# Performance work log

Measured on AMD Instinct MI355X. Metric: run time of the kernel, lower is better.

The kernel has to match this reference:

```python
import jax, jax.numpy as jnp
import numpy as np
import math

N_HEADS, INPUT_DIM, EMBED_DIM = 8, 128, 128
KEY_DIM = EMBED_DIM // N_HEADS  # val_dim = key_dim = 16
B, N = 4, 512


def setup_inputs() -> dict:
    key = jax.random.key(0)
    ks = jax.random.split(key, 8)
    stdv_k = 1.0 / math.sqrt(KEY_DIM)
    stdv_e = 1.0 / math.sqrt(EMBED_DIM)
    stdv_1 = 1.0
    q = jax.random.normal(ks[0], (B, N, INPUT_DIM), dtype=jnp.float32)
    e = jax.random.normal(ks[1], (B, N, N, INPUT_DIM), dtype=jnp.float32)
    W_query = jax.random.uniform(ks[2], (N_HEADS, INPUT_DIM, KEY_DIM), jnp.float32, -stdv_k, stdv_k)
    W_key = jax.random.uniform(ks[3], (N_HEADS, INPUT_DIM, KEY_DIM), jnp.float32, -stdv_k, stdv_k)
    W_val = jax.random.uniform(ks[4], (N_HEADS, INPUT_DIM, KEY_DIM), jnp.float32, -stdv_k, stdv_k)
    E_val1 = jax.random.uniform(ks[5], (N_HEADS, INPUT_DIM, 1), jnp.float32, -stdv_1, stdv_1)
    W_out = jax.random.uniform(ks[6], (N_HEADS, KEY_DIM, EMBED_DIM), jnp.float32, -stdv_e, stdv_e)
    return {"q": q, "e": e, "W_query": W_query, "W_key": W_key,
            "W_val": W_val, "E_val1": E_val1, "W_out": W_out}


def reference(q, e, W_query, W_key, W_val, E_val1, W_out):
    # h = q (self-attention); shapes: q [B,N,D], e [B,N,N,D]
    norm = 1.0 / math.sqrt(W_query.shape[-1])
    Q = jnp.einsum('bnd,hdk->hbnk', q, W_query)  # [H,B,N,k]
    K = jnp.einsum('bnd,hdk->hbnk', q, W_key)
    V = jnp.einsum('bnd,hdv->hbnv', q, W_val)
    # edge bias: per-head scalar projection of edge features -> [H,B,N,N]
    E = jnp.einsum('bnmd,hd->hbnm', e, E_val1[..., 0])
    compat = norm * jnp.einsum('hbnk,hbmk->hbnm', Q, K) + E
    attn = jax.nn.softmax(compat, axis=-1)
    heads = jnp.einsum('hbnm,hbmv->hbnv', attn, V)
    out = jnp.einsum('hbnv,hve->bne', heads, W_out)  # [B,N,embed]
    return out
```

## Files before the change

### kernel.cpp

```cpp
#include <hip/hip_runtime.h>
#include <math.h>

#define BB 4
#define NN 512
#define DD 128
#define HH 8
#define KK 16

typedef float f4 __attribute__((ext_vector_type(4)));

__device__ __forceinline__ f4 ntload4(const float* p) {
    return __builtin_nontemporal_load(reinterpret_cast<const f4*>(p));
}

__global__ __launch_bounds__(128) void proj_kernel(
    const float* __restrict__ q,
    const float* __restrict__ Wq,
    const float* __restrict__ Wk,
    const float* __restrict__ Wv,
    float* __restrict__ Qs,
    float* __restrict__ Kp,
    float* __restrict__ Vp)
{
    __shared__ float qrow[DD];
    const int bn = blockIdx.x;
    const int t = threadIdx.x;
    qrow[t] = q[(size_t)bn * DD + t];
    __syncthreads();
    const int h = t >> 4;
    const int k = t & 15;
    const float* wq = Wq + (size_t)h * DD * KK + k;
    const float* wk = Wk + (size_t)h * DD * KK + k;
    const float* wv = Wv + (size_t)h * DD * KK + k;
    float aq = 0.f, ak = 0.f, av = 0.f;
#pragma unroll 16
    for (int d = 0; d < DD; ++d) {
        const float x = qrow[d];
        aq = fmaf(x, wq[(size_t)d * KK], aq);
        ak = fmaf(x, wk[(size_t)d * KK], ak);
        av = fmaf(x, wv[(size_t)d * KK], av);
    }
    Qs[(size_t)bn * DD + t] = aq * 0.25f;
    Kp[(size_t)bn * DD + t] = ak;
    Vp[(size_t)bn * DD + t] = av;
}

__global__ __launch_bounds__(256) void vt_kernel(
    const float* __restrict__ Vp, float* __restrict__ Vt)
{
    __shared__ float tile[64][129];
    const int b  = blockIdx.x >> 3;
    const int m0 = (blockIdx.x & 7) * 64;
    const int t  = threadIdx.x;
    const float* src = Vp + ((size_t)b * NN + m0) * DD;
#pragma unroll
    for (int j = 0; j < 8; ++j) {
        const int idx4 = t + j * 256;
        const float4 v = *(const float4*)(src + (size_t)idx4 * 4);
        const int r = idx4 >> 5, c = (idx4 & 31) * 4;
        tile[r][c] = v.x; tile[r][c+1] = v.y; tile[r][c+2] = v.z; tile[r][c+3] = v.w;
    }
    __syncthreads();
    const int m = t & 63;
#pragma unroll
    for (int p0 = 0; p0 < 128; p0 += 4) {
        const int p = p0 + (t >> 6);
        Vt[((size_t)b * DD + p) * NN + m0 + m] = tile[m][p];
    }
}

__global__ __launch_bounds__(256) void qkt_kernel(
    const float* __restrict__ Qs, const float* __restrict__ Kp,
    float* __restrict__ QKT)
{
    const int b    = blockIdx.x >> 7;
    const int n4   = blockIdx.x & 127;
    const int tid  = threadIdx.x;
    const int wave = tid >> 6;
    const int lane = tid & 63;
    const int sub  = lane >> 4;
    const int dc   = lane & 15;
    const int d0   = dc * 8;

    float qf[4][8];
#pragma unroll
    for (int j = 0; j < 4; ++j) {
        const float* qp = Qs + ((size_t)b * NN + n4 * 4 + j) * DD + d0;
        const float4 a = *(const float4*)qp;
        const float4 c = *(const float4*)(qp + 4);
        qf[j][0]=a.x; qf[j][1]=a.y; qf[j][2]=a.z; qf[j][3]=a.w;
        qf[j][4]=c.x; qf[j][5]=c.y; qf[j][6]=c.z; qf[j][7]=c.w;
    }
    const float* kbase = Kp + (size_t)b * NN * DD;
    for (int i = 0; i < 32; ++i) {
        const int m = wave * 128 + i * 4 + sub;
        const float* kp = kbase + (size_t)m * DD + d0;
        const float4 k0 = *(const float4*)kp;
        const float4 k1 = *(const float4*)(kp + 4);
        float kr[8];
        kr[0]=k0.x; kr[1]=k0.y; kr[2]=k0.z; kr[3]=k0.w;
        kr[4]=k1.x; kr[5]=k1.y; kr[6]=k1.z; kr[7]=k1.w;
#pragma unroll
        for (int j = 0; j < 4; ++j) {
            float s = kr[0] * qf[j][0];
#pragma unroll
            for (int u = 1; u < 8; ++u) s = fmaf(kr[u], qf[j][u], s);
            s += __shfl_xor(s, 1);
            if ((dc & 1) == 0)
                QKT[(((size_t)b * NN + n4 * 4 + j) * HH + (dc >> 1)) * NN + m] = s;
        }
    }
}

__global__ __launch_bounds__(256) void ebias_kernel(
    const float* __restrict__ e,
    const float* __restrict__ Ev,
    float* __restrict__ E)
{
    const int tid  = threadIdx.x;
    const int wave = tid >> 6;
    const int lane = tid & 63;
    const int sub  = lane >> 4;
    const int dc   = lane & 15;
    const int d0   = dc * 8;
    const int W    = blockIdx.x * 4 + wave;

    float ev[HH][8];
#pragma unroll
    for (int h = 0; h < HH; ++h) {
        const float4 a = *(const float4*)(Ev + h * DD + d0);
        const float4 c = *(const float4*)(Ev + h * DD + d0 + 4);
        ev[h][0]=a.x; ev[h][1]=a.y; ev[h][2]=a.z; ev[h][3]=a.w;
        ev[h][4]=c.x; ev[h][5]=c.y; ev[h][6]=c.z; ev[h][7]=c.w;
    }
    const bool hi8 = (dc & 8) != 0;
    const bool hi4 = (dc & 4) != 0;
    const bool hi2 = (dc & 2) != 0;
    const int laneoff = sub * DD + d0;

    auto do_chunk = [&](const f4 e0, const f4 e1, const int C) {
        float er[8];
        er[0]=e0.x; er[1]=e0.y; er[2]=e0.z; er[3]=e0.w;
        er[4]=e1.x; er[5]=e1.y; er[6]=e1.z; er[7]=e1.w;
        float acc[HH];
#pragma unroll
        for (int h = 0; h < HH; ++h) {
            float s = er[0] * ev[h][0];
#pragma unroll
            for (int u = 1; u < 8; ++u) s = fmaf(er[u], ev[h][u], s);
            acc[h] = s;
        }
        float t4[4];
#pragma unroll
        for (int j = 0; j < 4; ++j) {
            const float keep = hi8 ? acc[j + 4] : acc[j];
            const float send = hi8 ? acc[j]     : acc[j + 4];
            t4[j] = keep + __shfl_xor(send, 8);
        }
        float t2[2];
#pragma unroll
        for (int j = 0; j < 2; ++j) {
            const float keep = hi4 ? t4[j + 2] : t4[j];
            const float send = hi4 ? t4[j]     : t4[j + 2];
            t2[j] = keep + __shfl_xor(send, 4);
        }
        float w;
        {
            const float keep = hi2 ? t2[1] : t2[0];
            const float send = hi2 ? t2[0] : t2[1];
            w = keep + __shfl_xor(send, 2);
        }
        w += __shfl_xor(w, 1);
        if ((dc & 1) == 0) {
            const int bn = C >> 7;
            const int m  = ((C & 127) << 2) + sub;
            E[((size_t)bn * HH + (dc >> 1)) * NN + m] = w;
        }
    };

#define LDE(B0, B1, p) { const float* _p = e + (size_t)(W + (p) * 8192) * 512 + laneoff; \
                         B0 = ntload4(_p); B1 = ntload4(_p + 4); }

    f4 A0, A1, B0, B1, C0, C1;
    LDE(A0, A1, 0); LDE(B0, B1, 1);
    for (int p = 0; p < 30; p += 3) {
        LDE(C0, C1, p + 2); do_chunk(A0, A1, W + p * 8192);
        LDE(A0, A1, p + 3); do_chunk(B0, B1, W + (p + 1) * 8192);
        LDE(B0, B1, p + 4); do_chunk(C0, C1, W + (p + 2) * 8192);
    }
    do_chunk(A0, A1, W + 30 * 8192); do_chunk(B0, B1, W + 31 * 8192);
#undef LDE
}

__global__ __launch_bounds__(256) void softmax_kernel(
    const float* __restrict__ E,
    const float* __restrict__ QKT,
    const float* __restrict__ Vt,
    const float* __restrict__ Wout,
    float* __restrict__ out)
{
    __shared__ float headsv[HH * KK];
    const int bn   = blockIdx.x;
    const int b    = bn >> 9;
    const int tid  = threadIdx.x;
    const int wave = tid >> 6;
    const int lane = tid & 63;

#pragma unroll
    for (int hh = 0; hh < 2; ++hh) {
        const int h = wave * 2 + hh;
        const float* eb   = E   + ((size_t)bn * HH + h) * NN;
        const float* qk   = QKT + ((size_t)bn * HH + h) * NN;
        const float* vrow = Vt + ((size_t)b * DD + h * KK) * NN;

        float s[8];
#pragma unroll
        for (int i = 0; i < 8; ++i)
            s[i] = eb[lane + i * 64] + qk[lane + i * 64];

        float mx = s[0];
#pragma unroll
        for (int i = 1; i < 8; ++i) mx = fmaxf(mx, s[i]);
#pragma unroll
        for (int mask = 1; mask <= 32; mask <<= 1)
            mx = fmaxf(mx, __shfl_xor(mx, mask));

        float pr[8], psum = 0.f;
#pragma unroll
        for (int i = 0; i < 8; ++i) { pr[i] = __expf(s[i] - mx); psum += pr[i]; }

        float av[KK];
#pragma unroll
        for (int v = 0; v < KK; ++v) av[v] = 0.f;
#pragma unroll
        for (int v = 0; v < KK; ++v) {
            const float* vp = vrow + (size_t)v * NN + lane;
#pragma unroll
            for (int i = 0; i < 8; ++i)
                av[v] = fmaf(pr[i], vp[i * 64], av[v]);
        }
#pragma unroll
        for (int mask = 1; mask <= 32; mask <<= 1)
            psum += __shfl_xor(psum, mask);

        const bool s5 = (lane & 32) != 0;
        float a8[8];
#pragma unroll
        for (int j = 0; j < 8; ++j) {
            const float keep = s5 ? av[j + 8] : av[j];
            const float send = s5 ? av[j]     : av[j + 8];
            a8[j] = keep + __shfl_xor(send, 32);
        }
        const bool s4 = (lane & 16) != 0;
        float a4[4];
#pragma unroll
        for (int j = 0; j < 4; ++j) {
            const float keep = s4 ? a8[j + 4] : a8[j];
            const float send = s4 ? a8[j]     : a8[j + 4];
            a4[j] = keep + __shfl_xor(send, 16);
        }
        const bool s3 = (lane & 8) != 0;
        float a2[2];
#pragma unroll
        for (int j = 0; j < 2; ++j) {
            const float keep = s3 ? a4[j + 2] : a4[j];
            const float send = s3 ? a4[j]     : a4[j + 2];
            a2[j] = keep + __shfl_xor(send, 8);
        }
        const bool s2 = (lane & 4) != 0;
        float a1;
        {
            const float keep = s2 ? a2[1] : a2[0];
            const float send = s2 ? a2[0] : a2[1];
            a1 = keep + __shfl_xor(send, 4);
        }
        a1 += __shfl_xor(a1, 2);
        a1 += __shfl_xor(a1, 1);
        if ((lane & 3) == 0)
            headsv[h * KK + (lane >> 2)] = a1 / psum;
    }
    __syncthreads();

    if (tid < DD) {
        float o = 0.f;
#pragma unroll 8
        for (int p = 0; p < HH * KK; ++p)
            o = fmaf(headsv[p], Wout[(size_t)p * DD + tid], o);
        out[(size_t)bn * DD + tid] = o;
    }
}

extern "C" void kernel_launch(void* const* d_in, const int* in_sizes, int n_in,
                              void* d_out, int out_size, void* d_ws, size_t ws_size,
                              hipStream_t stream) {
    const float* q    = (const float*)d_in[0];
    const float* e    = (const float*)d_in[1];
    const float* Wq   = (const float*)d_in[2];
    const float* Wk   = (const float*)d_in[3];
    const float* Wv   = (const float*)d_in[4];
    const float* Ev   = (const float*)d_in[5];
    const float* Wout = (const float*)d_in[6];
    float* out = (float*)d_out;

    float* Qs  = (float*)d_ws;
    float* Kp  = Qs  + (size_t)BB * NN * DD;
    float* Vp  = Kp  + (size_t)BB * NN * DD;
    float* Vt  = Vp  + (size_t)BB * NN * DD;
    float* QKT = Vt  + (size_t)BB * DD * NN;
    float* E   = QKT + (size_t)BB * NN * HH * NN;

    proj_kernel<<<BB * NN, 128, 0, stream>>>(q, Wq, Wk, Wv, Qs, Kp, Vp);
    vt_kernel<<<BB * 8, 256, 0, stream>>>(Vp, Vt);
    qkt_kernel<<<BB * 128, 256, 0, stream>>>(Qs, Kp, QKT);
    ebias_kernel<<<2048, 256, 0, stream>>>(e, Ev, E);
    softmax_kernel<<<BB * NN, 256, 0, stream>>>(E, QKT, Vt, Wout, out);
}
```

Baseline: 236.2 us.

## Compute edge bias projection with split-bf16 MFMA and one tile per wave

```diff
diff --git a/kernel.cpp b/kernel.cpp
--- a/kernel.cpp
+++ b/kernel.cpp
@@ -7,10 +7,31 @@
 #define HH 8
 #define KK 16
 
-typedef float f4 __attribute__((ext_vector_type(4)));
+typedef float f4     __attribute__((ext_vector_type(4)));
+typedef short bf16x8 __attribute__((ext_vector_type(8)));
 
 __device__ __forceinline__ f4 ntload4(const float* p) {
     return __builtin_nontemporal_load(reinterpret_cast<const f4*>(p));
+}
+
+__device__ __forceinline__ unsigned pack2(float lo, float hi) {
+    return (__float_as_uint(hi) & 0xFFFF0000u) | (__float_as_uint(lo) >> 16);
+}
+__device__ __forceinline__ bf16x8 packb(const f4 a, const f4 b) {
+    union { unsigned u[4]; bf16x8 v; } r;
+    r.u[0] = pack2(a.x, a.y);
+    r.u[1] = pack2(a.z, a.w);
+    r.u[2] = pack2(b.x, b.y);
+    r.u[3] = pack2(b.z, b.w);
+    return r.v;
+}
+__device__ __forceinline__ f4 hif(const f4 x) {
+    f4 r;
+    r.x = __uint_as_float(__float_as_uint(x.x) & 0xFFFF0000u);
+    r.y = __uint_as_float(__float_as_uint(x.y) & 0xFFFF0000u);
+    r.z = __uint_as_float(__float_as_uint(x.z) & 0xFFFF0000u);
+    r.w = __uint_as_float(__float_as_uint(x.w) & 0xFFFF0000u);
+    return r;
 }
 
 __global__ __launch_bounds__(128) void proj_kernel(
@@ -120,76 +141,50 @@
     const int tid  = threadIdx.x;
     const int wave = tid >> 6;
     const int lane = tid & 63;
-    const int sub  = lane >> 4;
-    const int dc   = lane & 15;
-    const int d0   = dc * 8;
     const int W    = blockIdx.x * 4 + wave;
-
-    float ev[HH][8];
-#pragma unroll
-    for (int h = 0; h < HH; ++h) {
-        const float4 a = *(const float4*)(Ev + h * DD + d0);
-        const float4 c = *(const float4*)(Ev + h * DD + d0 + 4);
-        ev[h][0]=a.x; ev[h][1]=a.y; ev[h][2]=a.z; ev[h][3]=a.w;
-        ev[h][4]=c.x; ev[h][5]=c.y; ev[h][6]=c.z; ev[h][7]=c.w;
-    }
-    const bool hi8 = (dc & 8) != 0;
-    const bool hi4 = (dc & 4) != 0;
-    const bool hi2 = (dc & 2) != 0;
-    const int laneoff = sub * DD + d0;
-
-    auto do_chunk = [&](const f4 e0, const f4 e1, const int C) {
-        float er[8];
-        er[0]=e0.x; er[1]=e0.y; er[2]=e0.z; er[3]=e0.w;
-        er[4]=e1.x; er[5]=e1.y; er[6]=e1.z; er[7]=e1.w;
-        float acc[HH];
-#pragma unroll
-        for (int h = 0; h < HH; ++h) {
-            float s = er[0] * ev[h][0];
-#pragma unroll
-            for (int u = 1; u < 8; ++u) s = fmaf(er[u], ev[h][u], s);
-            acc[h] = s;
-        }
-        float t4[4];
-#pragma unroll
-        for (int j = 0; j < 4; ++j) {
-            const float keep = hi8 ? acc[j + 4] : acc[j];
-            const float send = hi8 ? acc[j]     : acc[j + 4];
-            t4[j] = keep + __shfl_xor(send, 8);
-        }
-        float t2[2];
-#pragma unroll
-        for (int j = 0; j < 2; ++j) {
-            const float keep = hi4 ? t4[j + 2] : t4[j];
-            const float send = hi4 ? t4[j]     : t4[j + 2];
-            t2[j] = keep + __shfl_xor(send, 4);
-        }
-        float w;
-        {
-            const float keep = hi2 ? t2[1] : t2[0];
-            const float send = hi2 ? t2[0] : t2[1];
-            w = keep + __shfl_xor(send, 2);
-        }
-        w += __shfl_xor(w, 1);
-        if ((dc & 1) == 0) {
-            const int bn = C >> 7;
-            const int m  = ((C & 127) << 2) + sub;
-            E[((size_t)bn * HH + (dc >> 1)) * NN + m] = w;
-        }
-    };
-
-#define LDE(B0, B1, p) { const float* _p = e + (size_t)(W + (p) * 8192) * 512 + laneoff; \
-                         B0 = ntload4(_p); B1 = ntload4(_p + 4); }
-
-    f4 A0, A1, B0, B1, C0, C1;
-    LDE(A0, A1, 0); LDE(B0, B1, 1);
-    for (int p = 0; p < 30; p += 3) {
-        LDE(C0, C1, p + 2); do_chunk(A0, A1, W + p * 8192);
-        LDE(A0, A1, p + 3); do_chunk(B0, B1, W + (p + 1) * 8192);
-        LDE(B0, B1, p + 4); do_chunk(C0, C1, W + (p + 2) * 8192);
-    }
-    do_chunk(A0, A1, W + 30 * 8192); do_chunk(B0, B1, W + 31 * 8192);
-#undef LDE
+    const int bn   = W >> 5;
+    const int m0   = (W & 31) << 4;
+    const int row  = lane & 15;
+    const int kg   = lane >> 4;
+
+    bf16x8 Bhi[4], Blo[4];
+#pragma unroll
+    for (int s = 0; s < 4; ++s) {
+        f4 b0 = {0.f,0.f,0.f,0.f}, b1 = {0.f,0.f,0.f,0.f};
+        if (row < HH) {
+            const float* p = Ev + row * DD + s * 32 + kg * 8;
+            b0 = *(const f4*)p; b1 = *(const f4*)(p + 4);
+        }
+        Bhi[s] = packb(b0, b1);
+        const f4 l0 = b0 - hif(b0), l1 = b1 - hif(b1);
+        Blo[s] = packb(l0, l1);
+    }
+
+    const float* ab = e + ((size_t)bn * NN + m0 + row) * DD + kg * 8;
+    const f4 a00 = ntload4(ab +   0), a01 = ntload4(ab +   4);
+    const f4 a10 = ntload4(ab +  32), a11 = ntload4(ab +  36);
+    const f4 a20 = ntload4(ab +  64), a21 = ntload4(ab +  68);
+    const f4 a30 = ntload4(ab +  96), a31 = ntload4(ab + 100);
+
+    f4 acc = {0.f, 0.f, 0.f, 0.f};
+#define SLICE(A0, A1, s) {                                            \
+        const bf16x8 ahi = packb(A0, A1);                             \
+        const f4 lo0 = A0 - hif(A0), lo1 = A1 - hif(A1);              \
+        const bf16x8 alo = packb(lo0, lo1);                           \
+        acc = __builtin_amdgcn_mfma_f32_16x16x32_bf16(alo, Bhi[s], acc, 0, 0, 0); \
+        acc = __builtin_amdgcn_mfma_f32_16x16x32_bf16(ahi, Blo[s], acc, 0, 0, 0); \
+        acc = __builtin_amdgcn_mfma_f32_16x16x32_bf16(ahi, Bhi[s], acc, 0, 0, 0); \
+    }
+    SLICE(a00, a01, 0);
+    SLICE(a10, a11, 1);
+    SLICE(a20, a21, 2);
+    SLICE(a30, a31, 3);
+#undef SLICE
+
+    if (row < HH) {
+        float* dst = E + ((size_t)bn * HH + row) * NN + m0 + kg * 4;
+        *(f4*)dst = acc;
+    }
 }
 
 __global__ __launch_bounds__(256) void softmax_kernel(
@@ -312,6 +307,6 @@
     proj_kernel<<<BB * NN, 128, 0, stream>>>(q, Wq, Wk, Wv, Qs, Kp, Vp);
     vt_kernel<<<BB * 8, 256, 0, stream>>>(Vp, Vt);
     qkt_kernel<<<BB * 128, 256, 0, stream>>>(Qs, Kp, QKT);
-    ebias_kernel<<<2048, 256, 0, stream>>>(e, Ev, E);
+    ebias_kernel<<<BB * NN * NN / 64, 256, 0, stream>>>(e, Ev, E);
     softmax_kernel<<<BB * NN, 256, 0, stream>>>(E, QKT, Vt, Wout, out);
 }
```

Result: faster. 216.3 us (-8.4%).
